# Kernel tuning notes

Measured on AMD Instinct MI355X. Metric: run time of the kernel, lower is better.

Reference implementation:

```python
import jax, jax.numpy as jnp
import numpy as np
from functools import partial

EPS = 1e-5
TAU = 2.0
V_TH = 1.0
ALPHA = 4.0  # sigmoid surrogate sharpness (spikingjelly default)

@jax.custom_vjp
def heaviside(x):
    return (x >= 0.0).astype(x.dtype)

def _heaviside_fwd(x):
    return heaviside(x), x

def _heaviside_bwd(x, g):
    s = jax.nn.sigmoid(ALPHA * x)
    return (g * ALPHA * s * (1.0 - s),)

heaviside.defvjp(_heaviside_fwd, _heaviside_bwd)

def lif_multistep(x_seq):
    # x_seq: [T, ...]; LIF: v += (x - v)/tau; spike if v>=1; hard reset to 0 (detach_reset)
    def step(v, x):
        v = v + (x - v) / TAU
        spike = heaviside(v - V_TH)
        v = v * (1.0 - jax.lax.stop_gradient(spike))
        return v, spike
    _, spikes = jax.lax.scan(step, jnp.zeros_like(x_seq[0]), x_seq)
    return spikes

def bn_fold(g, b, m, v):
    scale = g * jax.lax.rsqrt(v + EPS)
    shift = b - m * scale
    return scale, shift

def setup_inputs() -> dict:
    key = jax.random.key(0)
    ks = jax.random.split(key, 11)
    T, B, C, H, W = 4, 32, 512, 32, 32
    HID, OUT = 64, 32
    return {
        "x": jax.random.normal(ks[0], (T, B, C, H, W), jnp.float32),
        "w1_w": jax.random.normal(ks[1], (HID, C), jnp.float32) * 0.05,
        "bn1_g": jax.random.uniform(ks[2], (HID,), jnp.float32, 0.5, 1.5),
        "bn1_b": jax.random.normal(ks[3], (HID,), jnp.float32) * 0.1,
        "bn1_m": jax.random.normal(ks[4], (HID,), jnp.float32) * 0.1,
        "bn1_v": jax.random.uniform(ks[5], (HID,), jnp.float32, 0.5, 1.5),
        "w2_w": jax.random.normal(ks[6], (OUT, HID), jnp.float32) * 0.1,
        "bn2_g": jax.random.uniform(ks[7], (OUT,), jnp.float32, 0.5, 1.5),
        "bn2_b": jax.random.normal(ks[8], (OUT,), jnp.float32) * 0.1,
        "bn2_m": jax.random.normal(ks[9], (OUT,), jnp.float32) * 0.1,
        "bn2_v": jax.random.uniform(ks[10], (OUT,), jnp.float32, 0.5, 1.5),
    }

def reference(x, w1_w, bn1_g, bn1_b, bn1_m, bn1_v, w2_w, bn2_g, bn2_b, bn2_m, bn2_v):
    T, B, C, H, W = x.shape
    N = H * W
    C_groups, L = 4, 8  # self.C=4, l=lidx+2=8; out_dim = C_groups*L
    xr = x.reshape(T, B, C, N)
    # conv1x1 + folded BN (inference)
    s1, sh1 = bn_fold(bn1_g, bn1_b, bn1_m, bn1_v)
    h = jnp.einsum('tbcn,oc->tbon', xr, w1_w)
    h = h * s1[:, None] + sh1[:, None]          # [T,B,HID,N]
    # spiking LIF temporal recurrence over T
    s = lif_multistep(h)                          # [T,B,HID,N]
    # conv1x1 + folded BN
    s2, sh2 = bn_fold(bn2_g, bn2_b, bn2_m, bn2_v)
    y = jnp.einsum('tbon,po->tbpn', s, w2_w)
    y = y * s2[:, None] + sh2[:, None]           # [T,B,OUT,N]
    # rearrange 'T B (C L) H W -> C T B L H W'
    dw = y.reshape(T, B, C_groups, L, H, W).transpose(2, 0, 1, 3, 4, 5)
    return dw
```

## Files before the change

### kernel.cpp

```cpp
#include <hip/hip_runtime.h>


#define T_   4
#define B_   32
#define C_   512
#define NPIX 1024
#define HID  64
#define OUTC 32
#define NT   64
#define CK   32
#define NCH  (C_ / CK)

typedef const __attribute__((address_space(1))) void* gas_t;
typedef __attribute__((address_space(3))) void* las_t;
typedef float v2f __attribute__((ext_vector_type(2)));

__global__ void w2_transpose(const float* __restrict__ w2, float* __restrict__ wst)
{
    const int o = threadIdx.x;
    #pragma unroll
    for (int p = 0; p < OUTC; ++p)
        wst[o * OUTC + p] = w2[p * HID + o];
}

__global__ __launch_bounds__(256, 2)
void snn_fused(const float* __restrict__ x,  const float* __restrict__ w1,
               const float* __restrict__ g1, const float* __restrict__ b1,
               const float* __restrict__ m1, const float* __restrict__ v1,
               const float* __restrict__ wst,
               const float* __restrict__ g2, const float* __restrict__ b2,
               const float* __restrict__ m2, const float* __restrict__ v2,
               float* __restrict__ out)
{
    __shared__ float xs[2][T_][CK][NT];
    __shared__ unsigned short spk[T_][4][NT];
    __shared__ float s2s[OUTC], sh2s[OUTC];

    const int tid = threadIdx.x;
    const int wv  = tid >> 6;
    const int ln  = tid & 63;
    const int b   = blockIdx.y;
    const int n0  = blockIdx.x * NT;
    const int wvu = __builtin_amdgcn_readfirstlane(wv);

    if (tid < OUTC) {
        float sc  = g2[tid] / sqrtf(v2[tid] + 1e-5f);
        s2s[tid]  = sc;
        sh2s[tid] = b2[tid] - m2[tid] * sc;
    }

    #define STAGE(ch, bf) do {                                                          \
        const int c0_ = (ch) * CK;                                                      \
        const float* gx_ = x + (((size_t)wv * B_ + b) * C_ + c0_) * NPIX + n0;          \
        _Pragma("unroll")                                                               \
        for (int j_ = 0; j_ < 8; ++j_) {                                                \
            const float* src_ = gx_ + (j_ * 4 + (ln >> 4)) * NPIX + ((ln & 15) << 2);   \
            __builtin_amdgcn_global_load_lds((gas_t)src_, (las_t)&xs[bf][wv][j_ * 4][0], 16, 0, 0); \
        }                                                                               \
    } while (0)

    v2f h01[16], h23[16];
    #pragma unroll
    for (int i = 0; i < 16; ++i) { h01[i] = (v2f){0.f, 0.f}; h23[i] = (v2f){0.f, 0.f}; }

    const float* w1u = w1 + (size_t)wvu * 16 * C_;

    STAGE(0, 0);
    __syncthreads();

    int bf = 0;
    for (int ch = 0; ch < NCH; ++ch) {
        if (ch + 1 < NCH) STAGE(ch + 1, bf ^ 1);
        const float* wc = w1u + ch * CK;
        #pragma unroll
        for (int c4 = 0; c4 < CK; c4 += 4) {
            v2f x01[4], x23[4];
            #pragma unroll
            for (int cc = 0; cc < 4; ++cc) {
                x01[cc] = (v2f){ xs[bf][0][c4 + cc][ln], xs[bf][1][c4 + cc][ln] };
                x23[cc] = (v2f){ xs[bf][2][c4 + cc][ln], xs[bf][3][c4 + cc][ln] };
            }
            #pragma unroll
            for (int i = 0; i < 16; ++i) {
                const float* wr = wc + i * C_ + c4;
                #pragma unroll
                for (int cc = 0; cc < 4; ++cc) {
                    const v2f ws = { wr[cc], wr[cc] };
                    h01[i] = __builtin_elementwise_fma(x01[cc], ws, h01[i]);
                    h23[i] = __builtin_elementwise_fma(x23[cc], ws, h23[i]);
                }
            }
        }
        __syncthreads();
        bf ^= 1;
    }

    {
        unsigned int msk[T_] = {0u, 0u, 0u, 0u};
        #pragma unroll
        for (int i = 0; i < 16; ++i) {
            const int o = wvu * 16 + i;
            const float sc = g1[o] / sqrtf(v1[o] + 1e-5f);
            const float sh = b1[o] - m1[o] * sc;
            const float hh[T_] = { h01[i].x, h01[i].y, h23[i].x, h23[i].y };
            float v = 0.f;
            #pragma unroll
            for (int t = 0; t < T_; ++t) {
                const float hb = hh[t] * sc + sh;
                v = v + (hb - v) * 0.5f;
                const bool sp = (v >= 1.0f);
                if (sp) msk[t] |= (1u << i);
                v = sp ? 0.f : v;
            }
        }
        #pragma unroll
        for (int t = 0; t < T_; ++t)
            spk[t][wv][ln] = (unsigned short)msk[t];
    }
    __syncthreads();

    {
        const int t = wv;
        const unsigned int mlo = (unsigned int)spk[t][0][ln] | ((unsigned int)spk[t][1][ln] << 16);
        const unsigned int mhi = (unsigned int)spk[t][2][ln] | ((unsigned int)spk[t][3][ln] << 16);

        v2f y2[16];
        #pragma unroll
        for (int p2 = 0; p2 < 16; ++p2) y2[p2] = (v2f){0.f, 0.f};

        #pragma unroll 8
        for (int o = 0; o < 32; ++o) {
            const float sp = (float)((mlo >> o) & 1u);
            const v2f spv = { sp, sp };
            const float* wr = wst + o * OUTC;
            #pragma unroll
            for (int p2 = 0; p2 < 16; ++p2)
                y2[p2] = __builtin_elementwise_fma(spv, ((const v2f*)wr)[p2], y2[p2]);
        }
        #pragma unroll 8
        for (int o = 0; o < 32; ++o) {
            const float sp = (float)((mhi >> o) & 1u);
            const v2f spv = { sp, sp };
            const float* wr = wst + (o + 32) * OUTC;
            #pragma unroll
            for (int p2 = 0; p2 < 16; ++p2)
                y2[p2] = __builtin_elementwise_fma(spv, ((const v2f*)wr)[p2], y2[p2]);
        }

        #pragma unroll
        for (int p2 = 0; p2 < 16; ++p2) {
            const float yy[2] = { y2[p2].x, y2[p2].y };
            #pragma unroll
            for (int k = 0; k < 2; ++k) {
                const int p  = p2 * 2 + k;
                const int cg = p >> 3, l = p & 7;
                const size_t idx = ((size_t)(((cg * T_ + t) * B_ + b) * 8 + l) << 10) + n0 + ln;
                out[idx] = yy[k] * s2s[p] + sh2s[p];
            }
        }
    }
    #undef STAGE
}

extern "C" void kernel_launch(void* const* d_in, const int* in_sizes, int n_in,
                              void* d_out, int out_size, void* d_ws, size_t ws_size,
                              hipStream_t stream)
{
    const float* x  = (const float*)d_in[0];
    const float* w1 = (const float*)d_in[1];
    const float* g1 = (const float*)d_in[2];
    const float* b1 = (const float*)d_in[3];
    const float* m1 = (const float*)d_in[4];
    const float* v1 = (const float*)d_in[5];
    const float* w2 = (const float*)d_in[6];
    const float* g2 = (const float*)d_in[7];
    const float* b2 = (const float*)d_in[8];
    const float* m2 = (const float*)d_in[9];
    const float* v2 = (const float*)d_in[10];

    float* wst = (float*)d_ws;

    w2_transpose<<<1, 64, 0, stream>>>(w2, wst);
    dim3 grid(NPIX / NT, B_);
    snn_fused<<<grid, 256, 0, stream>>>(x, w1, g1, b1, m1, v1, wst, g2, b2, m2, v2,
                                        (float*)d_out);
}
```

Before: 540.8 us.

## Assign each wave one timestep with all hidden channels, drop per-chunk barriers

```diff
diff --git a/kernel.cpp b/kernel.cpp
--- a/kernel.cpp
+++ b/kernel.cpp
@@ -15,24 +15,28 @@
 typedef __attribute__((address_space(3))) void* las_t;
 typedef float v2f __attribute__((ext_vector_type(2)));
 
-__global__ void w2_transpose(const float* __restrict__ w2, float* __restrict__ wst)
+__global__ void w_prep(const float* __restrict__ w1, const float* __restrict__ w2,
+                       float* __restrict__ w1t, float* __restrict__ w2t)
 {
-    const int o = threadIdx.x;
-    #pragma unroll
-    for (int p = 0; p < OUTC; ++p)
-        wst[o * OUTC + p] = w2[p * HID + o];
+    const int idx = blockIdx.x * 256 + threadIdx.x;
+    const int c = idx >> 6, o = idx & 63;
+    w1t[idx] = w1[o * C_ + c];
+    if (idx < HID * OUTC) {
+        const int oo = idx >> 5, p = idx & 31;
+        w2t[idx] = w2[p * HID + oo];
+    }
 }
 
 __global__ __launch_bounds__(256, 2)
-void snn_fused(const float* __restrict__ x,  const float* __restrict__ w1,
+void snn_fused(const float* __restrict__ x,  const float* __restrict__ w1t,
                const float* __restrict__ g1, const float* __restrict__ b1,
                const float* __restrict__ m1, const float* __restrict__ v1,
-               const float* __restrict__ wst,
+               const float* __restrict__ w2t,
                const float* __restrict__ g2, const float* __restrict__ b2,
                const float* __restrict__ m2, const float* __restrict__ v2,
                float* __restrict__ out)
 {
-    __shared__ float xs[2][T_][CK][NT];
+    __shared__ float pool[2 * T_ * CK * NT];
     __shared__ unsigned short spk[T_][4][NT];
     __shared__ float s2s[OUTC], sh2s[OUTC];
 
@@ -41,7 +45,6 @@
     const int ln  = tid & 63;
     const int b   = blockIdx.y;
     const int n0  = blockIdx.x * NT;
-    const int wvu = __builtin_amdgcn_readfirstlane(wv);
 
     if (tid < OUTC) {
         float sc  = g2[tid] / sqrtf(v2[tid] + 1e-5f);
@@ -49,64 +52,77 @@
         sh2s[tid] = b2[tid] - m2[tid] * sc;
     }
 
-    #define STAGE(ch, bf) do {                                                          \
+    float* xw0 = pool + (0 * T_ + wv) * CK * NT;
+    float* xw1 = pool + (1 * T_ + wv) * CK * NT;
+
+    #define STAGE(ch, dst) do {                                                         \
         const int c0_ = (ch) * CK;                                                      \
-        const float* gx_ = x + (((size_t)wv * B_ + b) * C_ + c0_) * NPIX + n0;          \
+        const float* gx_ = x + ((size_t)(wv * B_ + b) * C_ + c0_) * NPIX + n0;          \
         _Pragma("unroll")                                                               \
         for (int j_ = 0; j_ < 8; ++j_) {                                                \
             const float* src_ = gx_ + (j_ * 4 + (ln >> 4)) * NPIX + ((ln & 15) << 2);   \
-            __builtin_amdgcn_global_load_lds((gas_t)src_, (las_t)&xs[bf][wv][j_ * 4][0], 16, 0, 0); \
+            __builtin_amdgcn_global_load_lds((gas_t)src_, (las_t)((dst) + j_ * 4 * NT), 16, 0, 0); \
         }                                                                               \
     } while (0)
 
-    v2f h01[16], h23[16];
+    v2f acc2[32];
     #pragma unroll
-    for (int i = 0; i < 16; ++i) { h01[i] = (v2f){0.f, 0.f}; h23[i] = (v2f){0.f, 0.f}; }
-
-    const float* w1u = w1 + (size_t)wvu * 16 * C_;
-
-    STAGE(0, 0);
+    for (int q = 0; q < 32; ++q) acc2[q] = (v2f){0.f, 0.f};
+
+    STAGE(0, xw0);
+    asm volatile("s_waitcnt vmcnt(0)" ::: "memory");
+
+    float* xwc = xw0;
+    float* xwn = xw1;
+    for (int ch = 0; ch < NCH; ++ch) {
+        if (ch + 1 < NCH) STAGE(ch + 1, xwn);
+        const float* wc = w1t + (size_t)(ch * CK) * HID;
+        float xv[CK];
+        #pragma unroll
+        for (int c = 0; c < CK; ++c) xv[c] = xwc[c * NT + ln];
+        #pragma unroll
+        for (int c = 0; c < CK; ++c) {
+            const float* wr = wc + c * HID;
+            const v2f xsp = { xv[c], xv[c] };
+            #pragma unroll
+            for (int q = 0; q < 16; ++q) {
+                const float4 wq = *(const float4*)(wr + q * 4);
+                acc2[q * 2 + 0] = __builtin_elementwise_fma(xsp, (v2f){wq.x, wq.y}, acc2[q * 2 + 0]);
+                acc2[q * 2 + 1] = __builtin_elementwise_fma(xsp, (v2f){wq.z, wq.w}, acc2[q * 2 + 1]);
+            }
+        }
+        asm volatile("s_waitcnt vmcnt(0)" ::: "memory");
+        float* tmp = xwc; xwc = xwn; xwn = tmp;
+    }
+
+    #pragma unroll
+    for (int q = 0; q < 16; ++q) {
+        xw0[(2 * q + 0) * NT + ln] = acc2[q].x;
+        xw0[(2 * q + 1) * NT + ln] = acc2[q].y;
+        xw1[(2 * q + 0) * NT + ln] = acc2[16 + q].x;
+        xw1[(2 * q + 1) * NT + ln] = acc2[16 + q].y;
+    }
     __syncthreads();
 
-    int bf = 0;
-    for (int ch = 0; ch < NCH; ++ch) {
-        if (ch + 1 < NCH) STAGE(ch + 1, bf ^ 1);
-        const float* wc = w1u + ch * CK;
-        #pragma unroll
-        for (int c4 = 0; c4 < CK; c4 += 4) {
-            v2f x01[4], x23[4];
-            #pragma unroll
-            for (int cc = 0; cc < 4; ++cc) {
-                x01[cc] = (v2f){ xs[bf][0][c4 + cc][ln], xs[bf][1][c4 + cc][ln] };
-                x23[cc] = (v2f){ xs[bf][2][c4 + cc][ln], xs[bf][3][c4 + cc][ln] };
-            }
-            #pragma unroll
-            for (int i = 0; i < 16; ++i) {
-                const float* wr = wc + i * C_ + c4;
-                #pragma unroll
-                for (int cc = 0; cc < 4; ++cc) {
-                    const v2f ws = { wr[cc], wr[cc] };
-                    h01[i] = __builtin_elementwise_fma(x01[cc], ws, h01[i]);
-                    h23[i] = __builtin_elementwise_fma(x23[cc], ws, h23[i]);
-                }
-            }
-        }
-        __syncthreads();
-        bf ^= 1;
-    }
-
     {
+        float hr[16][T_];
+        #pragma unroll
+        for (int i = 0; i < 16; ++i) {
+            const int o = wv * 16 + i;
+            #pragma unroll
+            for (int t = 0; t < T_; ++t)
+                hr[i][t] = pool[(((o >> 5) * T_ + t) * CK + (o & 31)) * NT + ln];
+        }
         unsigned int msk[T_] = {0u, 0u, 0u, 0u};
         #pragma unroll
         for (int i = 0; i < 16; ++i) {
-            const int o = wvu * 16 + i;
+            const int o = wv * 16 + i;
             const float sc = g1[o] / sqrtf(v1[o] + 1e-5f);
             const float sh = b1[o] - m1[o] * sc;
-            const float hh[T_] = { h01[i].x, h01[i].y, h23[i].x, h23[i].y };
             float v = 0.f;
             #pragma unroll
             for (int t = 0; t < T_; ++t) {
-                const float hb = hh[t] * sc + sh;
+                const float hb = hr[i][t] * sc + sh;
                 v = v + (hb - v) * 0.5f;
                 const bool sp = (v >= 1.0f);
                 if (sp) msk[t] |= (1u << i);
@@ -132,7 +148,7 @@
         for (int o = 0; o < 32; ++o) {
             const float sp = (float)((mlo >> o) & 1u);
             const v2f spv = { sp, sp };
-            const float* wr = wst + o * OUTC;
+            const float* wr = w2t + o * OUTC;
             #pragma unroll
             for (int p2 = 0; p2 < 16; ++p2)
                 y2[p2] = __builtin_elementwise_fma(spv, ((const v2f*)wr)[p2], y2[p2]);
@@ -141,7 +157,7 @@
         for (int o = 0; o < 32; ++o) {
             const float sp = (float)((mhi >> o) & 1u);
             const v2f spv = { sp, sp };
-            const float* wr = wst + (o + 32) * OUTC;
+            const float* wr = w2t + (o + 32) * OUTC;
             #pragma unroll
             for (int p2 = 0; p2 < 16; ++p2)
                 y2[p2] = __builtin_elementwise_fma(spv, ((const v2f*)wr)[p2], y2[p2]);
@@ -178,10 +194,11 @@
     const float* m2 = (const float*)d_in[9];
     const float* v2 = (const float*)d_in[10];
 
-    float* wst = (float*)d_ws;
-
-    w2_transpose<<<1, 64, 0, stream>>>(w2, wst);
+    float* w1t = (float*)d_ws;
+    float* w2t = w1t + C_ * HID;
+
+    w_prep<<<128, 256, 0, stream>>>(w1, w2, w1t, w2t);
     dim3 grid(NPIX / NT, B_);
-    snn_fused<<<grid, 256, 0, stream>>>(x, w1, g1, b1, m1, v1, wst, g2, b2, m2, v2,
+    snn_fused<<<grid, 256, 0, stream>>>(x, w1t, g1, b1, m1, v1, w2t, g2, b2, m2, v2,
                                         (float*)d_out);
 }
```

Result: slower. 584.2 us (+8.0%).
